# Kernel optimization log

Hardware: AMD Instinct MI355X
Metric: run time of the kernel (lower is better)

Reference implementation:

```python
import jax, jax.numpy as jnp
import numpy as np

HIDDEN = 1024
B, S = 4, 2048


def setup_inputs() -> dict:
    key = jax.random.key(0)
    ks = jax.random.split(key, 9)
    scale = 1.0 / np.sqrt(HIDDEN)
    mk = lambda k: (jax.random.normal(k, (HIDDEN, HIDDEN), dtype=jnp.float32) * scale)
    return {
        "x": jax.random.normal(ks[0], (B, S, HIDDEN), dtype=jnp.float32),
        "Wq": mk(ks[1]), "bq": jnp.zeros((HIDDEN,), jnp.float32),
        "Wk": mk(ks[2]), "bk": jnp.zeros((HIDDEN,), jnp.float32),
        "Wv": mk(ks[3]), "bv": jnp.zeros((HIDDEN,), jnp.float32),
        "Wo": mk(ks[4]), "bo": jnp.zeros((HIDDEN,), jnp.float32),
    }


def reference(x, Wq, bq, Wk, bk, Wv, bv, Wo, bo):
    # Single-head attention over the full hidden dim (num_heads unused in source).
    # Linear(H,H): y = x @ W^T + b ; weights stored [out,in] torch-style.
    q = jnp.einsum("bsh,oh->bso", x, Wq) + bq  # [B,S,H]
    k = jnp.einsum("bsh,oh->bso", x, Wk) + bk
    v = jnp.einsum("bsh,oh->bso", x, Wv) + bv
    scores = jnp.einsum("bqh,bkh->bqk", q, k) / jnp.sqrt(jnp.float32(HIDDEN))
    attn = jax.nn.softmax(scores, axis=-1)  # dropout rate is 0.0 (eval-equivalent)
    ctx = jnp.einsum("bqk,bkh->bqh", attn, v)
    return jnp.einsum("bsh,oh->bso", ctx, Wo) + bo
```

## Files before the change

### kernel.cpp

```cpp
#include <hip/hip_runtime.h>

#define HID 1024
#define SEQ 2048
#define NB 4
#define BS 8192

typedef __attribute__((ext_vector_type(8))) short short8;
typedef __attribute__((ext_vector_type(8))) unsigned short ushort8;
typedef __attribute__((ext_vector_type(4))) float f32x4;

__device__ __forceinline__ float bf2f(unsigned short u) {
  unsigned int x = ((unsigned int)u) << 16;
  return __builtin_bit_cast(float, x);
}
__device__ __forceinline__ unsigned short f2bf(float f) {
  unsigned int x = __builtin_bit_cast(unsigned int, f);
  x = x + 0x7fffu + ((x >> 16) & 1u);
  return (unsigned short)(x >> 16);
}

#define GLOAD16(g, l)                                                          \
  __builtin_amdgcn_global_load_lds(                                            \
      (const __attribute__((address_space(1))) unsigned int*)(g),              \
      (__attribute__((address_space(3))) unsigned int*)(l), 16, 0, 0)

template <int N>
__device__ __forceinline__ void vmwait() {
  asm volatile("s_waitcnt vmcnt(%0)" ::"i"(N) : "memory");
}

__global__ void cast_f32_to_bf16(const float* __restrict__ in,
                                 unsigned short* __restrict__ out, int n) {
  int i = (blockIdx.x * 256 + threadIdx.x) * 8;
  if (i >= n) return;
  f32x4 a = *(const f32x4*)(in + i);
  f32x4 b = *(const f32x4*)(in + i + 4);
  ushort8 o;
  o[0] = f2bf(a[0]); o[1] = f2bf(a[1]); o[2] = f2bf(a[2]); o[3] = f2bf(a[3]);
  o[4] = f2bf(b[0]); o[5] = f2bf(b[1]); o[6] = f2bf(b[2]); o[7] = f2bf(b[3]);
  *(ushort8*)(out + i) = o;
}

__global__ __launch_bounds__(256) void transpose_cast(
    const float* __restrict__ in, unsigned short* __restrict__ out) {
  __shared__ float t[32][33];
  const int bx = blockIdx.x * 32, by = blockIdx.y * 32;
  const int tx = threadIdx.x & 31, ty = threadIdx.x >> 5;
#pragma unroll
  for (int i = 0; i < 4; ++i)
    t[ty + i * 8][tx] = in[(by + ty + i * 8) * 1024 + bx + tx];
  __syncthreads();
#pragma unroll
  for (int i = 0; i < 4; ++i)
    out[(bx + ty + i * 8) * 1024 + by + tx] = f2bf(t[tx][ty + i * 8]);
}

__global__ __launch_bounds__(256) void bias_fuse(const float* __restrict__ Wo,
                                                 const float* __restrict__ bv,
                                                 const float* __restrict__ bo,
                                                 float* __restrict__ bp) {
  const int h = blockIdx.x * 256 + threadIdx.x;
  float s = bo[h];
  for (int k = 0; k < 1024; ++k) s += Wo[h * 1024 + k] * bv[k];
  bp[h] = s;
}

template <int BN, int OUT_F32, int BIAS_MODE, int SWZ, int EPI>
__global__ __launch_bounds__(512, 2) void gemm8p(
    const unsigned short* __restrict__ A, const unsigned short* __restrict__ B,
    void* __restrict__ Cv, const float* __restrict__ bias,
    const float* __restrict__ bias2, float* __restrict__ Srow, int K, int lda,
    int ldb, int ldc, long long bsA, long long bsB, long long bsC,
    float alpha) {
  static_assert(BN == 256 || BN == 128, "BN");
  constexpr int WMW = (BN == 256) ? 2 : 4;
  constexpr int WNW = 8 / WMW;
  constexpr int MF = 8 / WMW;
  constexpr int NF = 2;
  constexpr int NBH = BN / 2;
  constexpr int GB = (BN == 256) ? 2 : 1;
  constexpr int BSLOT = NBH * 64;
  constexpr int WK0 = (BN == 256) ? 6 : 5;
  constexpr int WK3 = (BN == 256) ? 8 : 6;
  constexpr int WPR = (BN == 256) ? 4 : 3;

  __shared__ unsigned short ldsA[4 * 8192];
  __shared__ unsigned short ldsB[4 * BSLOT];

  const int tid = threadIdx.x;
  const int lane = tid & 63, wid = tid >> 6;
  const int fr = lane & 15, fq = lane >> 4;
  const int wm = wid / WNW, wn = wid % WNW;

  int bx, by, bz;
  if (SWZ == 1) {
    const int h = (blockIdx.z * 8 + blockIdx.y) * 8 + blockIdx.x;
    const int xcd = h & 7, j = h >> 3;
    const int zs = j / 32;
    bz = (xcd >> 1) + zs * 4;
    const int tile = (xcd & 1) * 32 + (j & 31);
    by = tile >> 3;
    bx = tile & 7;
  } else if (SWZ == 2) {
    const int nx = gridDim.x, nwg = nx * gridDim.y;
    int h = blockIdx.y * nx + blockIdx.x;
    int f = (h & 7) * (nwg >> 3) + (h >> 3);
    by = f % gridDim.y;
    bx = f / gridDim.y;
    bz = blockIdx.z;
  } else {
    const int nx = gridDim.x, nwg = nx * gridDim.y;
    int h = blockIdx.y * nx + blockIdx.x;
    int f = (h & 7) * (nwg >> 3) + (h >> 3);
    bx = f % nx;
    by = f / nx;
    bz = blockIdx.z;
  }

  const unsigned short* Ag = A + bz * bsA + (long long)by * 256 * lda;
  const unsigned short* Bg = B + bz * bsB + (long long)bx * BN * ldb;
  const int NT = K >> 6;

  const int La0 = wid * 1024 + lane * 16;
  const int La1 = 8192 + La0;
  const int Pa0 = La0 ^ ((La0 >> 4) & 0x70);
  const int Pa1 = La1 ^ ((La1 >> 4) & 0x70);
  const int aR0 = Pa0 >> 7, aC0 = (Pa0 & 127) >> 1;
  const int aR1 = Pa1 >> 7, aC1 = (Pa1 & 127) >> 1;

  auto stageA = [&](int tile, int h) {
    if (tile >= NT) return;
    unsigned short* d = &ldsA[(((tile & 1) << 1) | h) * 8192 + wid * 512];
    GLOAD16(Ag + (long long)(h * 128 + aR0) * lda + tile * 64 + aC0, d);
    GLOAD16(Ag + (long long)(h * 128 + aR1) * lda + tile * 64 + aC1, d + 4096);
  };
  auto stageB = [&](int tile, int h) {
    if (tile >= NT) return;
    unsigned short* d = &ldsB[(((tile & 1) << 1) | h) * BSLOT + wid * 512];
    GLOAD16(Bg + (long long)(h * NBH + aR0) * ldb + tile * 64 + aC0, d);
    if (GB == 2)
      GLOAD16(Bg + (long long)(h * NBH + aR1) * ldb + tile * 64 + aC1, d + 4096);
  };

  int offA[MF][2], offB[NF][2];
#pragma unroll
  for (int i = 0; i < MF; ++i)
#pragma unroll
    for (int s = 0; s < 2; ++s) {
      int b = (wm * (128 / WMW) + i * 16 + fr) * 128 + s * 64 + fq * 16;
      offA[i][s] = (b ^ ((b >> 4) & 0x70)) >> 1;
    }
#pragma unroll
  for (int n = 0; n < NF; ++n)
#pragma unroll
    for (int s = 0; s < 2; ++s) {
      int b = (wn * 32 + n * 16 + fr) * 128 + s * 64 + fq * 16;
      offB[n][s] = (b ^ ((b >> 4) & 0x70)) >> 1;
    }

  f32x4 acc[2][2][MF][NF] = {};

  stageA(0, 0); stageB(0, 0); stageA(0, 1); stageB(0, 1);
  stageA(1, 0); stageB(1, 0);
  vmwait<WPR>();
  __builtin_amdgcn_s_barrier();

  for (int kt = 0; kt < NT; kt += 2) {
    const bool tail = (kt + 2 >= NT);
#pragma unroll
    for (int t2 = 0; t2 < 2; ++t2) {
      const int buf = (kt + t2) & 1;
#pragma unroll
      for (int ph = 0; ph < 4; ++ph) {
        const int mh = ph >> 1, nh = ph & 1;
        const int p = t2 * 4 + ph;
        short8 av[MF][2], bw[NF][2];
        const unsigned short* pa = &ldsA[((buf << 1) | mh) * 8192];
        const unsigned short* pb = &ldsB[((buf << 1) | nh) * BSLOT];
#pragma unroll
        for (int i = 0; i < MF; ++i)
#pragma unroll
          for (int s = 0; s < 2; ++s)
            av[i][s] = *(const short8*)(pa + offA[i][s]);
#pragma unroll
        for (int n = 0; n < NF; ++n)
#pragma unroll
          for (int s = 0; s < 2; ++s)
            bw[n][s] = *(const short8*)(pb + offB[n][s]);
        if (p == 0) stageA(kt + 1, 1);
        else if (p == 1) stageB(kt + 1, 1);
        else if (p == 2) stageA(kt + 2, 0);
        else if (p == 3) stageB(kt + 2, 0);
        else if (p == 4) stageA(kt + 2, 1);
        else if (p == 5) stageB(kt + 2, 1);
        else if (p == 6) stageA(kt + 3, 0);
        else stageB(kt + 3, 0);
        __builtin_amdgcn_s_barrier();
        __builtin_amdgcn_s_setprio(1);
#pragma unroll
        for (int i = 0; i < MF; ++i)
#pragma unroll
          for (int n = 0; n < NF; ++n)
#pragma unroll
            for (int s = 0; s < 2; ++s)
              acc[mh][nh][i][n] = __builtin_amdgcn_mfma_f32_16x16x32_bf16(
                  av[i][s], bw[n][s], acc[mh][nh][i][n], 0, 0, 0);
        __builtin_amdgcn_s_setprio(0);
        if (p == 0) vmwait<WK0>();
        else if (p == 3) { if (tail) vmwait<0>(); else vmwait<WK3>(); }
        else if (p == 4) { if (tail) vmwait<0>(); else vmwait<WK0>(); }
        else if (p == 7) vmwait<WK3>();
        __builtin_amdgcn_s_barrier();
      }
    }
  }

  const long long cb0 = (long long)bz * bsC;
  float* sredf = (float*)ldsA;
#pragma unroll
  for (int mh = 0; mh < 2; ++mh)
#pragma unroll
    for (int i = 0; i < MF; ++i)
#pragma unroll
      for (int j = 0; j < 4; ++j) {
        const int row = mh * 128 + wm * (128 / WMW) + i * 16 + fq * 4 + j;
        float inv = 1.0f;
        if (EPI == 2) inv = 1.0f / Srow[(long long)bz * SEQ + by * 256 + row];
        float rps = 0.0f;
#pragma unroll
        for (int nh = 0; nh < 2; ++nh)
#pragma unroll
          for (int n = 0; n < NF; ++n) {
            const int col = bx * BN + nh * NBH + wn * 32 + n * 16 + fr;
            float v = acc[mh][nh][i][n][j] * alpha;
            if (EPI == 1) { v = __expf(v); rps += v; }
            if (EPI == 2) v *= inv;
            if (BIAS_MODE == 1) v += bias[col];
            if (BIAS_MODE == 3) v += (col < 1024) ? bias[col] : bias2[col - 1024];
            const long long idx =
                cb0 + (long long)(by * 256 + row) * ldc + col;
            if (OUT_F32)
              ((float*)Cv)[idx] = v;
            else
              ((unsigned short*)Cv)[idx] = f2bf(v);
          }
        if (EPI == 1) {
          rps += __shfl_xor(rps, 1, 64);
          rps += __shfl_xor(rps, 2, 64);
          rps += __shfl_xor(rps, 4, 64);
          rps += __shfl_xor(rps, 8, 64);
          if (fr == 0) sredf[row * WNW + wn] = rps;
        }
      }
  if (EPI == 1) {
    __syncthreads();
    if (tid < 256) {
      float s4 = 0.0f;
#pragma unroll
      for (int w = 0; w < WNW; ++w) s4 += sredf[tid * WNW + w];
      atomicAdd(Srow + (long long)bz * SEQ + by * 256 + tid, s4);
    }
  }
}

extern "C" void kernel_launch(void* const* d_in, const int* in_sizes, int n_in,
                              void* d_out, int out_size, void* d_ws,
                              size_t ws_size, hipStream_t stream) {
  (void)in_sizes; (void)n_in; (void)out_size; (void)ws_size;
  const float* x = (const float*)d_in[0];
  const float* Wq = (const float*)d_in[1];
  const float* bq = (const float*)d_in[2];
  const float* Wk = (const float*)d_in[3];
  const float* bk = (const float*)d_in[4];
  const float* Wv = (const float*)d_in[5];
  const float* bv = (const float*)d_in[6];
  const float* Wo = (const float*)d_in[7];
  const float* bo = (const float*)d_in[8];
  float* out = (float*)d_out;

  char* ws = (char*)d_ws;
  unsigned short* xbf  = (unsigned short*)(ws + 0);
  unsigned short* wqk  = (unsigned short*)(ws + 16777216);
  unsigned short* wobf = (unsigned short*)(ws + 20971520);
  unsigned short* wvT  = (unsigned short*)(ws + 23068672);
  unsigned short* wov  = (unsigned short*)(ws + 25165824);
  float*          bpr  = (float*)        (ws + 27262976);
  float*          Srow = (float*)        (ws + 28311552);
  unsigned short* VWoT = (unsigned short*)(ws + 33554432);
  unsigned short* QKb  = (unsigned short*)(ws + 50331648);
  unsigned short* P    = (unsigned short*)(ws + 83886080);

  cast_f32_to_bf16<<<4096, 256, 0, stream>>>(x, xbf, BS * HID);
  cast_f32_to_bf16<<<512, 256, 0, stream>>>(Wq, wqk, HID * HID);
  cast_f32_to_bf16<<<512, 256, 0, stream>>>(Wk, wqk + HID * HID, HID * HID);
  cast_f32_to_bf16<<<512, 256, 0, stream>>>(Wo, wobf, HID * HID);
  transpose_cast<<<dim3(32, 32), 256, 0, stream>>>(Wv, wvT);
  bias_fuse<<<4, 256, 0, stream>>>(Wo, bv, bo, bpr);
  hipMemsetAsync(Srow, 0, NB * SEQ * sizeof(float), stream);

  gemm8p<128, 0, 0, 0, 0><<<dim3(8, 4, 1), 512, 0, stream>>>(
      wobf, wvT, wov, nullptr, nullptr, nullptr, HID, HID, HID, HID, 0, 0, 0,
      1.0f);
  gemm8p<128, 0, 0, 2, 0><<<dim3(64, 4, 1), 512, 0, stream>>>(
      wov, xbf, VWoT, nullptr, nullptr, nullptr, HID, HID, HID, BS, 0, 0, 0,
      1.0f);
  gemm8p<256, 0, 3, 0, 0><<<dim3(8, 32, 1), 512, 0, stream>>>(
      xbf, wqk, QKb, bq, bk, nullptr, HID, HID, HID, 2048, 0, 0, 0, 1.0f);
  gemm8p<256, 0, 0, 1, 1><<<dim3(8, 8, NB), 512, 0, stream>>>(
      QKb, QKb + 1024, P, nullptr, nullptr, Srow, HID, 2048, 2048, SEQ,
      (long long)SEQ * 2048, (long long)SEQ * 2048, (long long)SEQ * SEQ,
      0.03125f);
  gemm8p<128, 1, 1, 1, 2><<<dim3(8, 8, NB), 512, 0, stream>>>(
      P, VWoT, out, bpr, nullptr, Srow, SEQ, SEQ, BS, HID,
      (long long)SEQ * SEQ, (long long)SEQ, (long long)SEQ * HID, 1.0f);
}
```

Before: 246.4 us.

## Replace 8-wave pipelined GEMM with smaller-tile double-buffered 4-wave GEMM

```diff
diff --git a/kernel.cpp b/kernel.cpp
--- a/kernel.cpp
+++ b/kernel.cpp
@@ -23,11 +23,6 @@
   __builtin_amdgcn_global_load_lds(                                            \
       (const __attribute__((address_space(1))) unsigned int*)(g),              \
       (__attribute__((address_space(3))) unsigned int*)(l), 16, 0, 0)
-
-template <int N>
-__device__ __forceinline__ void vmwait() {
-  asm volatile("s_waitcnt vmcnt(%0)" ::"i"(N) : "memory");
-}
 
 __global__ void cast_f32_to_bf16(const float* __restrict__ in,
                                  unsigned short* __restrict__ out, int n) {
@@ -59,206 +54,126 @@
                                                  const float* __restrict__ bv,
                                                  const float* __restrict__ bo,
                                                  float* __restrict__ bp) {
-  const int h = blockIdx.x * 256 + threadIdx.x;
-  float s = bo[h];
-  for (int k = 0; k < 1024; ++k) s += Wo[h * 1024 + k] * bv[k];
-  bp[h] = s;
-}
-
-template <int BN, int OUT_F32, int BIAS_MODE, int SWZ, int EPI>
-__global__ __launch_bounds__(512, 2) void gemm8p(
+  const int row = blockIdx.x * 4 + (threadIdx.x >> 6);
+  const int lane = threadIdx.x & 63;
+  float s = 0.f;
+  for (int k = lane; k < 1024; k += 64) s += Wo[row * 1024 + k] * bv[k];
+#pragma unroll
+  for (int off = 32; off >= 1; off >>= 1) s += __shfl_xor(s, off, 64);
+  if (lane == 0) bp[row] = s + bo[row];
+}
+
+template <int BN, int OUT_F32, int BIAS_MODE, int EPI>
+__global__ __launch_bounds__(256, 3) void gemm_tlp(
     const unsigned short* __restrict__ A, const unsigned short* __restrict__ B,
     void* __restrict__ Cv, const float* __restrict__ bias,
     const float* __restrict__ bias2, float* __restrict__ Srow, int K, int lda,
     int ldb, int ldc, long long bsA, long long bsB, long long bsC,
     float alpha) {
-  static_assert(BN == 256 || BN == 128, "BN");
-  constexpr int WMW = (BN == 256) ? 2 : 4;
-  constexpr int WNW = 8 / WMW;
-  constexpr int MF = 8 / WMW;
-  constexpr int NF = 2;
-  constexpr int NBH = BN / 2;
-  constexpr int GB = (BN == 256) ? 2 : 1;
-  constexpr int BSLOT = NBH * 64;
-  constexpr int WK0 = (BN == 256) ? 6 : 5;
-  constexpr int WK3 = (BN == 256) ? 8 : 6;
-  constexpr int WPR = (BN == 256) ? 4 : 3;
-
-  __shared__ unsigned short ldsA[4 * 8192];
-  __shared__ unsigned short ldsB[4 * BSLOT];
+  static_assert(BN == 128 || BN == 64, "BN");
+  constexpr int NF = BN / 32;
+  constexpr int CB = BN / 64;
+
+  __shared__ unsigned short lA[2][128 * 32];
+  __shared__ unsigned short lB[2][BN * 32];
 
   const int tid = threadIdx.x;
   const int lane = tid & 63, wid = tid >> 6;
   const int fr = lane & 15, fq = lane >> 4;
-  const int wm = wid / WNW, wn = wid % WNW;
-
-  int bx, by, bz;
-  if (SWZ == 1) {
-    const int h = (blockIdx.z * 8 + blockIdx.y) * 8 + blockIdx.x;
-    const int xcd = h & 7, j = h >> 3;
-    const int zs = j / 32;
-    bz = (xcd >> 1) + zs * 4;
-    const int tile = (xcd & 1) * 32 + (j & 31);
-    by = tile >> 3;
-    bx = tile & 7;
-  } else if (SWZ == 2) {
-    const int nx = gridDim.x, nwg = nx * gridDim.y;
-    int h = blockIdx.y * nx + blockIdx.x;
-    int f = (h & 7) * (nwg >> 3) + (h >> 3);
-    by = f % gridDim.y;
-    bx = f / gridDim.y;
-    bz = blockIdx.z;
-  } else {
-    const int nx = gridDim.x, nwg = nx * gridDim.y;
-    int h = blockIdx.y * nx + blockIdx.x;
-    int f = (h & 7) * (nwg >> 3) + (h >> 3);
-    bx = f % nx;
-    by = f / nx;
-    bz = blockIdx.z;
+  const int wm = wid >> 1, wn = wid & 1;
+
+  const int nx = gridDim.x;
+  const int nwg = nx * gridDim.y;
+  int f = blockIdx.y * nx + blockIdx.x;
+  f = (f & 7) * (nwg >> 3) + (f >> 3);
+  const int bx = f % nx, by = f / nx;
+  const int bz = blockIdx.z;
+
+  const unsigned short* Ag = A + bz * bsA + (long long)by * 128 * lda;
+  const unsigned short* Bg = B + bz * bsB + (long long)bx * BN * ldb;
+  const int NT = K >> 5;
+
+  const int srow = tid >> 2, scol = (tid & 3) * 8;
+  const int lbase = wid * 512;
+
+  auto stageA = [&](int t) {
+    unsigned short* d0 = &lA[t & 1][lbase];
+    GLOAD16(Ag + (long long)srow * lda + t * 32 + scol, d0);
+    GLOAD16(Ag + (long long)(64 + srow) * lda + t * 32 + scol, d0 + 2048);
+  };
+  auto stageB = [&](int t) {
+    unsigned short* d0 = &lB[t & 1][lbase];
+    GLOAD16(Bg + (long long)srow * ldb + t * 32 + scol, d0);
+    if (CB == 2)
+      GLOAD16(Bg + (long long)(64 + srow) * ldb + t * 32 + scol, d0 + 2048);
+  };
+
+  f32x4 acc[4][NF] = {};
+
+  stageA(0);
+  stageB(0);
+  __syncthreads();
+
+  for (int t = 0; t < NT; ++t) {
+    if (t + 1 < NT) {
+      stageA(t + 1);
+      stageB(t + 1);
+    }
+    const unsigned short* pa = lA[t & 1];
+    const unsigned short* pb = lB[t & 1];
+    short8 av[4], bw[NF];
+#pragma unroll
+    for (int i = 0; i < 4; ++i)
+      av[i] = *(const short8*)(pa + (wm * 64 + i * 16 + fr) * 32 + fq * 8);
+#pragma unroll
+    for (int n = 0; n < NF; ++n)
+      bw[n] = *(const short8*)(pb + (wn * (BN / 2) + n * 16 + fr) * 32 + fq * 8);
+#pragma unroll
+    for (int i = 0; i < 4; ++i)
+#pragma unroll
+      for (int n = 0; n < NF; ++n)
+        acc[i][n] = __builtin_amdgcn_mfma_f32_16x16x32_bf16(av[i], bw[n],
+                                                            acc[i][n], 0, 0, 0);
+    __syncthreads();
   }
 
-  const unsigned short* Ag = A + bz * bsA + (long long)by * 256 * lda;
-  const unsigned short* Bg = B + bz * bsB + (long long)bx * BN * ldb;
-  const int NT = K >> 6;
-
-  const int La0 = wid * 1024 + lane * 16;
-  const int La1 = 8192 + La0;
-  const int Pa0 = La0 ^ ((La0 >> 4) & 0x70);
-  const int Pa1 = La1 ^ ((La1 >> 4) & 0x70);
-  const int aR0 = Pa0 >> 7, aC0 = (Pa0 & 127) >> 1;
-  const int aR1 = Pa1 >> 7, aC1 = (Pa1 & 127) >> 1;
-
-  auto stageA = [&](int tile, int h) {
-    if (tile >= NT) return;
-    unsigned short* d = &ldsA[(((tile & 1) << 1) | h) * 8192 + wid * 512];
-    GLOAD16(Ag + (long long)(h * 128 + aR0) * lda + tile * 64 + aC0, d);
-    GLOAD16(Ag + (long long)(h * 128 + aR1) * lda + tile * 64 + aC1, d + 4096);
-  };
-  auto stageB = [&](int tile, int h) {
-    if (tile >= NT) return;
-    unsigned short* d = &ldsB[(((tile & 1) << 1) | h) * BSLOT + wid * 512];
-    GLOAD16(Bg + (long long)(h * NBH + aR0) * ldb + tile * 64 + aC0, d);
-    if (GB == 2)
-      GLOAD16(Bg + (long long)(h * NBH + aR1) * ldb + tile * 64 + aC1, d + 4096);
-  };
-
-  int offA[MF][2], offB[NF][2];
-#pragma unroll
-  for (int i = 0; i < MF; ++i)
-#pragma unroll
-    for (int s = 0; s < 2; ++s) {
-      int b = (wm * (128 / WMW) + i * 16 + fr) * 128 + s * 64 + fq * 16;
-      offA[i][s] = (b ^ ((b >> 4) & 0x70)) >> 1;
-    }
-#pragma unroll
-  for (int n = 0; n < NF; ++n)
-#pragma unroll
-    for (int s = 0; s < 2; ++s) {
-      int b = (wn * 32 + n * 16 + fr) * 128 + s * 64 + fq * 16;
-      offB[n][s] = (b ^ ((b >> 4) & 0x70)) >> 1;
-    }
-
-  f32x4 acc[2][2][MF][NF] = {};
-
-  stageA(0, 0); stageB(0, 0); stageA(0, 1); stageB(0, 1);
-  stageA(1, 0); stageB(1, 0);
-  vmwait<WPR>();
-  __builtin_amdgcn_s_barrier();
-
-  for (int kt = 0; kt < NT; kt += 2) {
-    const bool tail = (kt + 2 >= NT);
-#pragma unroll
-    for (int t2 = 0; t2 < 2; ++t2) {
-      const int buf = (kt + t2) & 1;
-#pragma unroll
-      for (int ph = 0; ph < 4; ++ph) {
-        const int mh = ph >> 1, nh = ph & 1;
-        const int p = t2 * 4 + ph;
-        short8 av[MF][2], bw[NF][2];
-        const unsigned short* pa = &ldsA[((buf << 1) | mh) * 8192];
-        const unsigned short* pb = &ldsB[((buf << 1) | nh) * BSLOT];
-#pragma unroll
-        for (int i = 0; i < MF; ++i)
-#pragma unroll
-          for (int s = 0; s < 2; ++s)
-            av[i][s] = *(const short8*)(pa + offA[i][s]);
-#pragma unroll
-        for (int n = 0; n < NF; ++n)
-#pragma unroll
-          for (int s = 0; s < 2; ++s)
-            bw[n][s] = *(const short8*)(pb + offB[n][s]);
-        if (p == 0) stageA(kt + 1, 1);
-        else if (p == 1) stageB(kt + 1, 1);
-        else if (p == 2) stageA(kt + 2, 0);
-        else if (p == 3) stageB(kt + 2, 0);
-        else if (p == 4) stageA(kt + 2, 1);
-        else if (p == 5) stageB(kt + 2, 1);
-        else if (p == 6) stageA(kt + 3, 0);
-        else stageB(kt + 3, 0);
-        __builtin_amdgcn_s_barrier();
-        __builtin_amdgcn_s_setprio(1);
-#pragma unroll
-        for (int i = 0; i < MF; ++i)
-#pragma unroll
-          for (int n = 0; n < NF; ++n)
-#pragma unroll
-            for (int s = 0; s < 2; ++s)
-              acc[mh][nh][i][n] = __builtin_amdgcn_mfma_f32_16x16x32_bf16(
-                  av[i][s], bw[n][s], acc[mh][nh][i][n], 0, 0, 0);
-        __builtin_amdgcn_s_setprio(0);
-        if (p == 0) vmwait<WK0>();
-        else if (p == 3) { if (tail) vmwait<0>(); else vmwait<WK3>(); }
-        else if (p == 4) { if (tail) vmwait<0>(); else vmwait<WK0>(); }
-        else if (p == 7) vmwait<WK3>();
-        __builtin_amdgcn_s_barrier();
+  const long long cb0 = (long long)bz * bsC;
+  float* sredf = (float*)lA;
+#pragma unroll
+  for (int i = 0; i < 4; ++i)
+#pragma unroll
+    for (int j = 0; j < 4; ++j) {
+      const int row = wm * 64 + i * 16 + fq * 4 + j;
+      float inv = 1.0f;
+      if (EPI == 2) inv = 1.0f / Srow[(long long)bz * SEQ + by * 128 + row];
+      float rps = 0.0f;
+#pragma unroll
+      for (int n = 0; n < NF; ++n) {
+        const int col = bx * BN + wn * (BN / 2) + n * 16 + fr;
+        float v = acc[i][n][j] * alpha;
+        if (EPI == 1) { v = __expf(v); rps += v; }
+        if (EPI == 2) v *= inv;
+        if (BIAS_MODE == 1) v += bias[col];
+        if (BIAS_MODE == 3) v += (col < 1024) ? bias[col] : bias2[col - 1024];
+        const long long idx = cb0 + (long long)(by * 128 + row) * ldc + col;
+        if (OUT_F32)
+          ((float*)Cv)[idx] = v;
+        else
+          ((unsigned short*)Cv)[idx] = f2bf(v);
+      }
+      if (EPI == 1) {
+        rps += __shfl_xor(rps, 1, 64);
+        rps += __shfl_xor(rps, 2, 64);
+        rps += __shfl_xor(rps, 4, 64);
+        rps += __shfl_xor(rps, 8, 64);
+        if (fr == 0) sredf[row * 2 + wn] = rps;
       }
     }
-  }
-
-  const long long cb0 = (long long)bz * bsC;
-  float* sredf = (float*)ldsA;
-#pragma unroll
-  for (int mh = 0; mh < 2; ++mh)
-#pragma unroll
-    for (int i = 0; i < MF; ++i)
-#pragma unroll
-      for (int j = 0; j < 4; ++j) {
-        const int row = mh * 128 + wm * (128 / WMW) + i * 16 + fq * 4 + j;
-        float inv = 1.0f;
-        if (EPI == 2) inv = 1.0f / Srow[(long long)bz * SEQ + by * 256 + row];
-        float rps = 0.0f;
-#pragma unroll
-        for (int nh = 0; nh < 2; ++nh)
-#pragma unroll
-          for (int n = 0; n < NF; ++n) {
-            const int col = bx * BN + nh * NBH + wn * 32 + n * 16 + fr;
-            float v = acc[mh][nh][i][n][j] * alpha;
-            if (EPI == 1) { v = __expf(v); rps += v; }
-            if (EPI == 2) v *= inv;
-            if (BIAS_MODE == 1) v += bias[col];
-            if (BIAS_MODE == 3) v += (col < 1024) ? bias[col] : bias2[col - 1024];
-            const long long idx =
-                cb0 + (long long)(by * 256 + row) * ldc + col;
-            if (OUT_F32)
-              ((float*)Cv)[idx] = v;
-            else
-              ((unsigned short*)Cv)[idx] = f2bf(v);
-          }
-        if (EPI == 1) {
-          rps += __shfl_xor(rps, 1, 64);
-          rps += __shfl_xor(rps, 2, 64);
-          rps += __shfl_xor(rps, 4, 64);
-          rps += __shfl_xor(rps, 8, 64);
-          if (fr == 0) sredf[row * WNW + wn] = rps;
-        }
-      }
   if (EPI == 1) {
     __syncthreads();
-    if (tid < 256) {
-      float s4 = 0.0f;
-#pragma unroll
-      for (int w = 0; w < WNW; ++w) s4 += sredf[tid * WNW + w];
-      atomicAdd(Srow + (long long)bz * SEQ + by * 256 + tid, s4);
+    if (tid < 128) {
+      const float s2 = sredf[tid * 2] + sredf[tid * 2 + 1];
+      atomicAdd(Srow + (long long)bz * SEQ + by * 128 + tid, s2);
     }
   }
 }
@@ -295,22 +210,22 @@
   cast_f32_to_bf16<<<512, 256, 0, stream>>>(Wk, wqk + HID * HID, HID * HID);
   cast_f32_to_bf16<<<512, 256, 0, stream>>>(Wo, wobf, HID * HID);
   transpose_cast<<<dim3(32, 32), 256, 0, stream>>>(Wv, wvT);
-  bias_fuse<<<4, 256, 0, stream>>>(Wo, bv, bo, bpr);
+  bias_fuse<<<256, 256, 0, stream>>>(Wo, bv, bo, bpr);
   hipMemsetAsync(Srow, 0, NB * SEQ * sizeof(float), stream);
 
-  gemm8p<128, 0, 0, 0, 0><<<dim3(8, 4, 1), 512, 0, stream>>>(
+  gemm_tlp<128, 0, 0, 0><<<dim3(8, 8, 1), 256, 0, stream>>>(
       wobf, wvT, wov, nullptr, nullptr, nullptr, HID, HID, HID, HID, 0, 0, 0,
       1.0f);
-  gemm8p<128, 0, 0, 2, 0><<<dim3(64, 4, 1), 512, 0, stream>>>(
+  gemm_tlp<64, 0, 0, 0><<<dim3(128, 8, 1), 256, 0, stream>>>(
       wov, xbf, VWoT, nullptr, nullptr, nullptr, HID, HID, HID, BS, 0, 0, 0,
       1.0f);
-  gemm8p<256, 0, 3, 0, 0><<<dim3(8, 32, 1), 512, 0, stream>>>(
+  gemm_tlp<128, 0, 3, 0><<<dim3(16, 64, 1), 256, 0, stream>>>(
       xbf, wqk, QKb, bq, bk, nullptr, HID, HID, HID, 2048, 0, 0, 0, 1.0f);
-  gemm8p<256, 0, 0, 1, 1><<<dim3(8, 8, NB), 512, 0, stream>>>(
+  gemm_tlp<128, 0, 0, 1><<<dim3(16, 16, NB), 256, 0, stream>>>(
       QKb, QKb + 1024, P, nullptr, nullptr, Srow, HID, 2048, 2048, SEQ,
       (long long)SEQ * 2048, (long long)SEQ * 2048, (long long)SEQ * SEQ,
       0.03125f);
-  gemm8p<128, 1, 1, 1, 2><<<dim3(8, 8, NB), 512, 0, stream>>>(
+  gemm_tlp<64, 1, 1, 2><<<dim3(16, 16, NB), 256, 0, stream>>>(
       P, VWoT, out, bpr, nullptr, Srow, SEQ, SEQ, BS, HID,
       (long long)SEQ * SEQ, (long long)SEQ, (long long)SEQ * HID, 1.0f);
 }
```

New measurement: 234.5 us. 1.05x faster.
